# Kernel tuning notes

Measured on AMD Instinct MI355X. Metric: run time of the kernel, lower is better.

Reference implementation:

```python
import jax, jax.numpy as jnp
import numpy as np
import math

H_DIM = 1024
N_HEADS = 16
B, T = 2, 2048


def setup_inputs() -> dict:
    key = jax.random.key(0)
    ks = jax.random.split(key, 9)
    scale = 1.0 / math.sqrt(H_DIM)
    x = jax.random.normal(ks[0], (B, T, H_DIM), dtype=jnp.float32)
    Wq = jax.random.normal(ks[1], (H_DIM, H_DIM), dtype=jnp.float32) * scale
    Wk = jax.random.normal(ks[2], (H_DIM, H_DIM), dtype=jnp.float32) * scale
    Wv = jax.random.normal(ks[3], (H_DIM, H_DIM), dtype=jnp.float32) * scale
    Wp = jax.random.normal(ks[4], (H_DIM, H_DIM), dtype=jnp.float32) * scale
    bq = jnp.zeros((H_DIM,), dtype=jnp.float32)
    bk = jnp.zeros((H_DIM,), dtype=jnp.float32)
    bv = jnp.zeros((H_DIM,), dtype=jnp.float32)
    bp = jnp.zeros((H_DIM,), dtype=jnp.float32)
    return {"x": x, "Wq": Wq, "bq": bq, "Wk": Wk, "bk": bk,
            "Wv": Wv, "bv": bv, "Wp": Wp, "bp": bp}


def _attention(x, Wq, bq, Wk, bk, Wv, bv, Wp, bp):
    Bx, Tx, C = x.shape
    N = N_HEADS
    D = C // N
    # torch Linear: x @ W.T + b
    q = (x @ Wq.T + bq).reshape(Bx, Tx, N, D).transpose(0, 2, 1, 3)  # [B,N,T,D]
    k = (x @ Wk.T + bk).reshape(Bx, Tx, N, D).transpose(0, 2, 1, 3)
    v = (x @ Wv.T + bv).reshape(Bx, Tx, N, D).transpose(0, 2, 1, 3)
    scores = jnp.einsum('bntd,bnsd->bnts', q, k) / math.sqrt(D)  # [B,N,T,T]
    causal = jnp.tril(jnp.ones((Tx, Tx), dtype=bool))
    scores = jnp.where(causal[None, None], scores, -jnp.inf)
    probs = jax.nn.softmax(scores, axis=-1)
    attn = jnp.einsum('bnts,bnsd->bntd', probs, v)  # [B,N,T,D]
    attn = attn.transpose(0, 2, 1, 3).reshape(Bx, Tx, C)
    return attn @ Wp.T + bp


def reference(x, Wq, bq, Wk, bk, Wv, bv, Wp, bp):
    return _attention(x, Wq, bq, Wk, bk, Wv, bv, Wp, bp)
```

## Files before the change

kernel.cpp:

```cpp
#include <hip/hip_runtime.h>
#include <hip/hip_bf16.h>
#include <math.h>

#define TSEQ 2048
#define CDIM 1024
#define NHEADS 16
#define DHEAD 64
#define BSZ 2
#define MROWS (BSZ * TSEQ)
#define SCALE_Q 0.18033688f

typedef __attribute__((ext_vector_type(8))) short short8;
typedef __attribute__((ext_vector_type(4))) short short4v;
typedef __attribute__((ext_vector_type(4))) float f32x4;

__device__ inline f32x4 mfma16(short8 a, short8 b, f32x4 c) {
    return __builtin_amdgcn_mfma_f32_16x16x32_bf16(a, b, c, 0, 0, 0);
}

__device__ inline short f2bf(float f) {
    __hip_bfloat16 h = __float2bfloat16(f);
    return __builtin_bit_cast(short, h);
}

__global__ __launch_bounds__(256) void convx_kernel(const float* __restrict__ x,
                                                    short* __restrict__ xb) {
    size_t off = (size_t)(blockIdx.x * 256 + threadIdx.x) * 8;
    float4 a = *(const float4*)(x + off);
    float4 b = *(const float4*)(x + off + 4);
    short8 h;
    h[0] = f2bf(a.x); h[1] = f2bf(a.y); h[2] = f2bf(a.z); h[3] = f2bf(a.w);
    h[4] = f2bf(b.x); h[5] = f2bf(b.y); h[6] = f2bf(b.z); h[7] = f2bf(b.w);
    *(short8*)(xb + off) = h;
}

__global__ __launch_bounds__(256, 3) void gemm_qkv(
    const short* __restrict__ xb, const float* __restrict__ Wq,
    const float* __restrict__ Wk, const float* __restrict__ Wv,
    const float* __restrict__ bq, const float* __restrict__ bk,
    const float* __restrict__ bv, short* __restrict__ qws,
    short* __restrict__ kws, short* __restrict__ vtws) {
    __shared__ __attribute__((aligned(16))) short a_lds[128][72];
    __shared__ __attribute__((aligned(16))) short b_lds[128][72];

    const int tid = threadIdx.x;
    const int lane = tid & 63;
    const int wv = tid >> 6;
    const int wr = wv >> 1, wc = wv & 1;
    const int l15 = lane & 15, l4 = lane >> 4;
    const int mbase = blockIdx.x * 128;
    const int which = blockIdx.y >> 3;
    const int nbase = (blockIdx.y & 7) * 128;
    const float* Wf = which == 0 ? Wq : (which == 1 ? Wk : Wv);
    const float* bias = which == 0 ? bq : (which == 1 ? bk : bv);

    f32x4 acc[4][4];
#pragma unroll
    for (int i = 0; i < 4; ++i)
#pragma unroll
        for (int j = 0; j < 4; ++j) acc[i][j] = f32x4{0.f, 0.f, 0.f, 0.f};

    const int ar = tid >> 3;
    const int ag = (tid & 7) * 8;
    const int br = tid >> 4;
    const int bg = (tid & 15) * 4;
    const short* aptr = xb + (size_t)(mbase + ar) * CDIM + ag;
    const float* bptr = Wf + (size_t)(nbase + br) * CDIM + bg;

    short8 apre[4];
    float4 bpre[8];
#pragma unroll
    for (int it = 0; it < 4; ++it)
        apre[it] = *(const short8*)(aptr + (size_t)(32 * it) * CDIM);
#pragma unroll
    for (int it = 0; it < 8; ++it)
        bpre[it] = *(const float4*)(bptr + (size_t)(16 * it) * CDIM);

    for (int k0 = 0; k0 < CDIM; k0 += 64) {
        __syncthreads();
#pragma unroll
        for (int it = 0; it < 4; ++it)
            *(short8*)&a_lds[ar + 32 * it][ag] = apre[it];
#pragma unroll
        for (int it = 0; it < 8; ++it) {
            short4v h;
            h.x = f2bf(bpre[it].x); h.y = f2bf(bpre[it].y);
            h.z = f2bf(bpre[it].z); h.w = f2bf(bpre[it].w);
            *(short4v*)&b_lds[br + 16 * it][bg] = h;
        }
        __syncthreads();
        if (k0 + 64 < CDIM) {
#pragma unroll
            for (int it = 0; it < 4; ++it)
                apre[it] = *(const short8*)(aptr + (size_t)(32 * it) * CDIM + k0 + 64);
#pragma unroll
            for (int it = 0; it < 8; ++it)
                bpre[it] = *(const float4*)(bptr + (size_t)(16 * it) * CDIM + k0 + 64);
        }

#pragma unroll
        for (int kk = 0; kk < 2; ++kk) {
            short8 af[4], bfr[4];
#pragma unroll
            for (int i = 0; i < 4; ++i)
                af[i] = *(const short8*)&a_lds[wr * 64 + i * 16 + l15][kk * 32 + l4 * 8];
#pragma unroll
            for (int j = 0; j < 4; ++j)
                bfr[j] = *(const short8*)&b_lds[wc * 64 + j * 16 + l15][kk * 32 + l4 * 8];
#pragma unroll
            for (int i = 0; i < 4; ++i)
#pragma unroll
                for (int j = 0; j < 4; ++j)
                    acc[i][j] = mfma16(af[i], bfr[j], acc[i][j]);
        }
    }

    if (which < 2) {
        short* dst = which == 0 ? qws : kws;
        const float scale = which == 0 ? SCALE_Q : 1.0f;
#pragma unroll
        for (int i = 0; i < 4; ++i) {
            int mrow = mbase + wr * 64 + i * 16 + l4 * 4;
#pragma unroll
            for (int j = 0; j < 4; ++j) {
                int o = nbase + wc * 64 + j * 16 + l15;
                int n = o >> 6, d = o & 63;
                float bval = bias[o];
#pragma unroll
                for (int r = 0; r < 4; ++r) {
                    int mm = mrow + r;
                    int bb = mm >> 11;
                    int t = mm & (TSEQ - 1);
                    dst[(((size_t)bb * NHEADS + n) * TSEQ + t) * DHEAD + d] =
                        f2bf((acc[i][j][r] + bval) * scale);
                }
            }
        }
    } else {
#pragma unroll
        for (int i = 0; i < 4; ++i) {
            int mrow = mbase + wr * 64 + i * 16 + l4 * 4;
            int bb = mrow >> 11;
            int t = mrow & (TSEQ - 1);
#pragma unroll
            for (int j = 0; j < 4; ++j) {
                int o = nbase + wc * 64 + j * 16 + l15;
                int n = o >> 6, d = o & 63;
                float bval = bias[o];
                short4v h4;
#pragma unroll
                for (int r = 0; r < 4; ++r) h4[r] = f2bf(acc[i][j][r] + bval);
                *(short4v*)&vtws[(((size_t)bb * NHEADS + n) * DHEAD + d) * TSEQ + t] = h4;
            }
        }
    }
}

__global__ __launch_bounds__(256) void gemm_p(
    const short* __restrict__ attn, const float* __restrict__ Wp,
    const float* __restrict__ bp, float* __restrict__ out) {
    __shared__ __attribute__((aligned(16))) short a_lds[64][40];
    __shared__ __attribute__((aligned(16))) short b_lds[128][40];

    const int tid = threadIdx.x;
    const int lane = tid & 63;
    const int wv = tid >> 6;
    const int wr = wv >> 1, wc = wv & 1;
    const int l15 = lane & 15, l4 = lane >> 4;
    const int mbase = blockIdx.x * 64;
    const int nbase = blockIdx.y * 128;

    f32x4 acc[2][4];
#pragma unroll
    for (int i = 0; i < 2; ++i)
#pragma unroll
        for (int j = 0; j < 4; ++j) acc[i][j] = f32x4{0.f, 0.f, 0.f, 0.f};

    const int arow = tid >> 2;
    const int acol = (tid & 3) * 8;
    const int brow = tid >> 3;
    const int bcol = (tid & 7) * 4;
    const short* aptr = attn + (size_t)(mbase + arow) * CDIM + acol;
    const float* bptr = Wp + (size_t)(nbase + brow) * CDIM + bcol;

    short8 apre;
    float4 bpre[4];
    apre = *(const short8*)(aptr);
#pragma unroll
    for (int it = 0; it < 4; ++it)
        bpre[it] = *(const float4*)(bptr + (size_t)(it * 32) * CDIM);

    for (int k0 = 0; k0 < CDIM; k0 += 32) {
        __syncthreads();
        *(short8*)&a_lds[arow][acol] = apre;
#pragma unroll
        for (int it = 0; it < 4; ++it) {
            short4v h;
            h.x = f2bf(bpre[it].x); h.y = f2bf(bpre[it].y);
            h.z = f2bf(bpre[it].z); h.w = f2bf(bpre[it].w);
            *(short4v*)&b_lds[brow + it * 32][bcol] = h;
        }
        __syncthreads();
        if (k0 + 32 < CDIM) {
            apre = *(const short8*)(aptr + k0 + 32);
#pragma unroll
            for (int it = 0; it < 4; ++it)
                bpre[it] = *(const float4*)(bptr + (size_t)(it * 32) * CDIM + k0 + 32);
        }

        short8 af[2], bfr[4];
#pragma unroll
        for (int i = 0; i < 2; ++i)
            af[i] = *(const short8*)&a_lds[wr * 32 + i * 16 + l15][l4 * 8];
#pragma unroll
        for (int j = 0; j < 4; ++j)
            bfr[j] = *(const short8*)&b_lds[wc * 64 + j * 16 + l15][l4 * 8];
#pragma unroll
        for (int i = 0; i < 2; ++i)
#pragma unroll
            for (int j = 0; j < 4; ++j)
                acc[i][j] = mfma16(af[i], bfr[j], acc[i][j]);
    }

#pragma unroll
    for (int i = 0; i < 2; ++i) {
        int mrow = mbase + wr * 32 + i * 16 + l4 * 4;
#pragma unroll
        for (int j = 0; j < 4; ++j) {
            int o = nbase + wc * 64 + j * 16 + l15;
            float bval = bp[o];
#pragma unroll
            for (int r = 0; r < 4; ++r)
                out[(size_t)(mrow + r) * CDIM + o] = acc[i][j][r] + bval;
        }
    }
}

__global__ __launch_bounds__(256) void attn_kernel(
    const short* __restrict__ q, const short* __restrict__ k,
    const short* __restrict__ vt, short* __restrict__ attn_out) {
    __shared__ __attribute__((aligned(16))) short k_lds[64][64];
    __shared__ __attribute__((aligned(16))) short vt_lds[64][64];
    __shared__ __attribute__((aligned(16))) short p_lds[4][16][80];

    const int tid = threadIdx.x;
    const int w = tid >> 6;
    const int lane = tid & 63;
    const int l15 = lane & 15;
    const int l4 = lane >> 4;
    const int h = blockIdx.x;
    const int qtile = gridDim.y - 1 - blockIdx.y;
    const int qb = qtile * 64;
    const int wrow0 = qb + w * 16;

    short8 qf[2];
#pragma unroll
    for (int kh = 0; kh < 2; ++kh)
        qf[kh] = *(const short8*)(q + ((size_t)h * TSEQ + wrow0 + l15) * DHEAD +
                                  kh * 32 + l4 * 8);

    float l_run[4];
    f32x4 o_acc[4];
#pragma unroll
    for (int r = 0; r < 4; ++r) l_run[r] = 0.f;
#pragma unroll
    for (int dt = 0; dt < 4; ++dt) o_acc[dt] = f32x4{0.f, 0.f, 0.f, 0.f};

    const int ntiles = qtile + 1;
    const int srow = tid >> 3;
    const int sgrp = tid & 7;

    short8 kpre[2], vpre[2];
#pragma unroll
    for (int it = 0; it < 2; ++it) {
        int row = srow + it * 32;
        kpre[it] = *(const short8*)(k + ((size_t)h * TSEQ + row) * DHEAD + sgrp * 8);
        vpre[it] = *(const short8*)(vt + ((size_t)h * DHEAD + row) * TSEQ + sgrp * 8);
    }

    for (int kvt = 0; kvt < ntiles; ++kvt) {
        const int kvbase = kvt * 64;
        __syncthreads();
#pragma unroll
        for (int it = 0; it < 2; ++it) {
            int row = srow + it * 32;
            int gs = sgrp ^ (row & 7);
            *(short8*)&k_lds[row][gs * 8] = kpre[it];
            *(short8*)&vt_lds[row][gs * 8] = vpre[it];
        }
        __syncthreads();
        if (kvt + 1 < ntiles) {
            int kvb2 = kvbase + 64;
#pragma unroll
            for (int it = 0; it < 2; ++it) {
                int row = srow + it * 32;
                kpre[it] = *(const short8*)(k + ((size_t)h * TSEQ + kvb2 + row) * DHEAD + sgrp * 8);
                vpre[it] = *(const short8*)(vt + ((size_t)h * DHEAD + row) * TSEQ + kvb2 + sgrp * 8);
            }
        }

        f32x4 s[4];
#pragma unroll
        for (int jt = 0; jt < 4; ++jt) {
            int row = jt * 16 + l15;
            int sw = row & 7;
            short8 kf0 = *(const short8*)&k_lds[row][(l4 ^ sw) * 8];
            short8 kf1 = *(const short8*)&k_lds[row][((4 + l4) ^ sw) * 8];
            f32x4 a = f32x4{0.f, 0.f, 0.f, 0.f};
            a = mfma16(qf[0], kf0, a);
            a = mfma16(qf[1], kf1, a);
            s[jt] = a;
        }

        const bool needmask = (kvbase + 63 > wrow0);
#pragma unroll
        for (int r = 0; r < 4; ++r) {
            int qrow = wrow0 + l4 * 4 + r;
            float lp = 0.f;
#pragma unroll
            for (int jt = 0; jt < 4; ++jt) {
                float x = s[jt][r];
                if (needmask && (kvbase + jt * 16 + l15 > qrow)) x = -INFINITY;
                float e = __builtin_amdgcn_exp2f(x);
                lp += e;
                p_lds[w][l4 * 4 + r][jt * 16 + l15] = f2bf(e);
            }
            l_run[r] += lp;
        }

        short8 pa0 = *(const short8*)&p_lds[w][l15][l4 * 8];
        short8 pa1 = *(const short8*)&p_lds[w][l15][32 + l4 * 8];
#pragma unroll
        for (int dt = 0; dt < 4; ++dt) {
            int row = dt * 16 + l15;
            int sw = row & 7;
            short8 vf0 = *(const short8*)&vt_lds[row][(l4 ^ sw) * 8];
            short8 vf1 = *(const short8*)&vt_lds[row][((4 + l4) ^ sw) * 8];
            o_acc[dt] = mfma16(pa0, vf0, o_acc[dt]);
            o_acc[dt] = mfma16(pa1, vf1, o_acc[dt]);
        }
    }

#pragma unroll
    for (int r = 0; r < 4; ++r) {
        float l = l_run[r];
#pragma unroll
        for (int mk = 1; mk < 16; mk <<= 1) l += __shfl_xor(l, mk);
        l_run[r] = 1.0f / l;
    }
    const int b = h >> 4, n = h & 15;
#pragma unroll
    for (int dt = 0; dt < 4; ++dt) {
#pragma unroll
        for (int r = 0; r < 4; ++r) {
            int t = wrow0 + l4 * 4 + r;
            attn_out[((size_t)b * TSEQ + t) * CDIM + n * DHEAD + dt * 16 + l15] =
                f2bf(o_acc[dt][r] * l_run[r]);
        }
    }
}

extern "C" void kernel_launch(void* const* d_in, const int* in_sizes, int n_in,
                              void* d_out, int out_size, void* d_ws, size_t ws_size,
                              hipStream_t stream) {
    const float* x  = (const float*)d_in[0];
    const float* Wq = (const float*)d_in[1];
    const float* bq = (const float*)d_in[2];
    const float* Wk = (const float*)d_in[3];
    const float* bk = (const float*)d_in[4];
    const float* Wv = (const float*)d_in[5];
    const float* bv = (const float*)d_in[6];
    const float* Wp = (const float*)d_in[7];
    const float* bp = (const float*)d_in[8];

    char* ws = (char*)d_ws;
    const size_t SZ = (size_t)MROWS * CDIM * sizeof(short);
    short* qws  = (short*)(ws);
    short* kws  = (short*)(ws + SZ);
    short* vtws = (short*)(ws + 2 * SZ);
    short* xb   = (short*)(ws + 3 * SZ);
    short* attn = xb;

    convx_kernel<<<2048, 256, 0, stream>>>(x, xb);
    gemm_qkv<<<dim3(MROWS / 128, 24), 256, 0, stream>>>(xb, Wq, Wk, Wv, bq, bk, bv,
                                                         qws, kws, vtws);
    attn_kernel<<<dim3(BSZ * NHEADS, TSEQ / 64), 256, 0, stream>>>(qws, kws, vtws, attn);
    gemm_p<<<dim3(MROWS / 64, CDIM / 128), 256, 0, stream>>>(attn, Wp, bp, (float*)d_out);
}
```

Measured before the change: 117.3 us.

## Widen attention KV tile to 128 and pre-convert Wp to bf16

The attention kernel now processes 128 keys per iteration instead of 64. This halves the loop trips and barriers per query tile, using larger LDS buffers with a 16-way swizzle on V. Separately, Wp is converted to bf16 by a convx launch into the now-free q workspace, so gemm_p loads bf16 tiles directly instead of converting fp32 inside the K loop. In exchange there is an extra kernel launch, more LDS and registers in attention, and extra masked work on the diagonal tile.

```diff
diff --git a/kernel.cpp b/kernel.cpp
--- a/kernel.cpp
+++ b/kernel.cpp
@@ -157,7 +157,7 @@
 }
 
 __global__ __launch_bounds__(256) void gemm_p(
-    const short* __restrict__ attn, const float* __restrict__ Wp,
+    const short* __restrict__ attn, const short* __restrict__ wpb,
     const float* __restrict__ bp, float* __restrict__ out) {
     __shared__ __attribute__((aligned(16))) short a_lds[64][40];
     __shared__ __attribute__((aligned(16))) short b_lds[128][40];
@@ -178,34 +178,24 @@
 
     const int arow = tid >> 2;
     const int acol = (tid & 3) * 8;
-    const int brow = tid >> 3;
-    const int bcol = (tid & 7) * 4;
     const short* aptr = attn + (size_t)(mbase + arow) * CDIM + acol;
-    const float* bptr = Wp + (size_t)(nbase + brow) * CDIM + bcol;
-
-    short8 apre;
-    float4 bpre[4];
+    const short* bptr = wpb + (size_t)(nbase + arow) * CDIM + acol;
+
+    short8 apre, bpre[2];
     apre = *(const short8*)(aptr);
-#pragma unroll
-    for (int it = 0; it < 4; ++it)
-        bpre[it] = *(const float4*)(bptr + (size_t)(it * 32) * CDIM);
+    bpre[0] = *(const short8*)(bptr);
+    bpre[1] = *(const short8*)(bptr + (size_t)64 * CDIM);
 
     for (int k0 = 0; k0 < CDIM; k0 += 32) {
         __syncthreads();
         *(short8*)&a_lds[arow][acol] = apre;
-#pragma unroll
-        for (int it = 0; it < 4; ++it) {
-            short4v h;
-            h.x = f2bf(bpre[it].x); h.y = f2bf(bpre[it].y);
-            h.z = f2bf(bpre[it].z); h.w = f2bf(bpre[it].w);
-            *(short4v*)&b_lds[brow + it * 32][bcol] = h;
-        }
+        *(short8*)&b_lds[arow][acol] = bpre[0];
+        *(short8*)&b_lds[arow + 64][acol] = bpre[1];
         __syncthreads();
         if (k0 + 32 < CDIM) {
             apre = *(const short8*)(aptr + k0 + 32);
-#pragma unroll
-            for (int it = 0; it < 4; ++it)
-                bpre[it] = *(const float4*)(bptr + (size_t)(it * 32) * CDIM + k0 + 32);
+            bpre[0] = *(const short8*)(bptr + k0 + 32);
+            bpre[1] = *(const short8*)(bptr + (size_t)64 * CDIM + k0 + 32);
         }
 
         short8 af[2], bfr[4];
@@ -239,9 +229,9 @@
 __global__ __launch_bounds__(256) void attn_kernel(
     const short* __restrict__ q, const short* __restrict__ k,
     const short* __restrict__ vt, short* __restrict__ attn_out) {
-    __shared__ __attribute__((aligned(16))) short k_lds[64][64];
-    __shared__ __attribute__((aligned(16))) short vt_lds[64][64];
-    __shared__ __attribute__((aligned(16))) short p_lds[4][16][80];
+    __shared__ __attribute__((aligned(16))) short k_lds[128][64];
+    __shared__ __attribute__((aligned(16))) short vt_lds[64][128];
+    __shared__ __attribute__((aligned(16))) short p_lds[4][16][136];
 
     const int tid = threadIdx.x;
     const int w = tid >> 6;
@@ -250,8 +240,7 @@
     const int l4 = lane >> 4;
     const int h = blockIdx.x;
     const int qtile = gridDim.y - 1 - blockIdx.y;
-    const int qb = qtile * 64;
-    const int wrow0 = qb + w * 16;
+    const int wrow0 = qtile * 64 + w * 16;
 
     short8 qf[2];
 #pragma unroll
@@ -266,42 +255,43 @@
 #pragma unroll
     for (int dt = 0; dt < 4; ++dt) o_acc[dt] = f32x4{0.f, 0.f, 0.f, 0.f};
 
-    const int ntiles = qtile + 1;
-    const int srow = tid >> 3;
-    const int sgrp = tid & 7;
-
-    short8 kpre[2], vpre[2];
-#pragma unroll
-    for (int it = 0; it < 2; ++it) {
-        int row = srow + it * 32;
-        kpre[it] = *(const short8*)(k + ((size_t)h * TSEQ + row) * DHEAD + sgrp * 8);
-        vpre[it] = *(const short8*)(vt + ((size_t)h * DHEAD + row) * TSEQ + sgrp * 8);
+    const int ntiles = (qtile + 2) >> 1;
+    const size_t kbase = (size_t)h * TSEQ * DHEAD;
+    const size_t vbase = (size_t)h * DHEAD * TSEQ;
+
+    const int ksrow = tid >> 3, ksg = tid & 7;
+    const int vsrow = tid >> 4, vsg = tid & 15;
+
+    short8 kpre[4], vpre[4];
+#pragma unroll
+    for (int it = 0; it < 4; ++it) {
+        kpre[it] = *(const short8*)(k + kbase + (size_t)(ksrow + it * 32) * DHEAD + ksg * 8);
+        vpre[it] = *(const short8*)(vt + vbase + (size_t)(vsrow + it * 16) * TSEQ + vsg * 8);
     }
 
     for (int kvt = 0; kvt < ntiles; ++kvt) {
-        const int kvbase = kvt * 64;
-        __syncthreads();
-#pragma unroll
-        for (int it = 0; it < 2; ++it) {
-            int row = srow + it * 32;
-            int gs = sgrp ^ (row & 7);
-            *(short8*)&k_lds[row][gs * 8] = kpre[it];
-            *(short8*)&vt_lds[row][gs * 8] = vpre[it];
+        const int kvbase = kvt * 128;
+        __syncthreads();
+#pragma unroll
+        for (int it = 0; it < 4; ++it) {
+            int krow = ksrow + it * 32;
+            *(short8*)&k_lds[krow][(ksg ^ (krow & 7)) * 8] = kpre[it];
+            int vrow = vsrow + it * 16;
+            *(short8*)&vt_lds[vrow][((vsg ^ (vrow & 15))) * 8] = vpre[it];
         }
         __syncthreads();
         if (kvt + 1 < ntiles) {
-            int kvb2 = kvbase + 64;
-#pragma unroll
-            for (int it = 0; it < 2; ++it) {
-                int row = srow + it * 32;
-                kpre[it] = *(const short8*)(k + ((size_t)h * TSEQ + kvb2 + row) * DHEAD + sgrp * 8);
-                vpre[it] = *(const short8*)(vt + ((size_t)h * DHEAD + row) * TSEQ + kvb2 + sgrp * 8);
-            }
-        }
-
-        f32x4 s[4];
-#pragma unroll
-        for (int jt = 0; jt < 4; ++jt) {
+            int kvb2 = kvbase + 128;
+#pragma unroll
+            for (int it = 0; it < 4; ++it) {
+                kpre[it] = *(const short8*)(k + kbase + (size_t)(kvb2 + ksrow + it * 32) * DHEAD + ksg * 8);
+                vpre[it] = *(const short8*)(vt + vbase + (size_t)(vsrow + it * 16) * TSEQ + kvb2 + vsg * 8);
+            }
+        }
+
+        f32x4 s[8];
+#pragma unroll
+        for (int jt = 0; jt < 8; ++jt) {
             int row = jt * 16 + l15;
             int sw = row & 7;
             short8 kf0 = *(const short8*)&k_lds[row][(l4 ^ sw) * 8];
@@ -312,13 +302,13 @@
             s[jt] = a;
         }
 
-        const bool needmask = (kvbase + 63 > wrow0);
+        const bool needmask = (kvbase + 127 > wrow0);
 #pragma unroll
         for (int r = 0; r < 4; ++r) {
             int qrow = wrow0 + l4 * 4 + r;
             float lp = 0.f;
 #pragma unroll
-            for (int jt = 0; jt < 4; ++jt) {
+            for (int jt = 0; jt < 8; ++jt) {
                 float x = s[jt][r];
                 if (needmask && (kvbase + jt * 16 + l15 > qrow)) x = -INFINITY;
                 float e = __builtin_amdgcn_exp2f(x);
@@ -328,16 +318,19 @@
             l_run[r] += lp;
         }
 
-        short8 pa0 = *(const short8*)&p_lds[w][l15][l4 * 8];
-        short8 pa1 = *(const short8*)&p_lds[w][l15][32 + l4 * 8];
+        short8 pa[4];
+#pragma unroll
+        for (int ks = 0; ks < 4; ++ks)
+            pa[ks] = *(const short8*)&p_lds[w][l15][ks * 32 + l4 * 8];
 #pragma unroll
         for (int dt = 0; dt < 4; ++dt) {
             int row = dt * 16 + l15;
-            int sw = row & 7;
-            short8 vf0 = *(const short8*)&vt_lds[row][(l4 ^ sw) * 8];
-            short8 vf1 = *(const short8*)&vt_lds[row][((4 + l4) ^ sw) * 8];
-            o_acc[dt] = mfma16(pa0, vf0, o_acc[dt]);
-            o_acc[dt] = mfma16(pa1, vf1, o_acc[dt]);
+            int sw = row & 15;
+#pragma unroll
+            for (int ks = 0; ks < 4; ++ks) {
+                short8 vf = *(const short8*)&vt_lds[row][((ks * 4 + l4) ^ sw) * 8];
+                o_acc[dt] = mfma16(pa[ks], vf, o_acc[dt]);
+            }
         }
     }
 
@@ -380,10 +373,12 @@
     short* vtws = (short*)(ws + 2 * SZ);
     short* xb   = (short*)(ws + 3 * SZ);
     short* attn = xb;
+    short* wpb  = qws;
 
     convx_kernel<<<2048, 256, 0, stream>>>(x, xb);
     gemm_qkv<<<dim3(MROWS / 128, 24), 256, 0, stream>>>(xb, Wq, Wk, Wv, bq, bk, bv,
                                                          qws, kws, vtws);
     attn_kernel<<<dim3(BSZ * NHEADS, TSEQ / 64), 256, 0, stream>>>(qws, kws, vtws, attn);
-    gemm_p<<<dim3(MROWS / 64, CDIM / 128), 256, 0, stream>>>(attn, Wp, bp, (float*)d_out);
-}
+    convx_kernel<<<512, 256, 0, stream>>>(Wp, wpb);
+    gemm_p<<<dim3(MROWS / 64, CDIM / 128), 256, 0, stream>>>(attn, wpb, bp, (float*)d_out);
+}
```

New measurement: 112.9 us. 1.04x faster.
